# Kernel optimization log

Measured on AMD Instinct MI355X. Metric: run time of the kernel, lower is better.

The kernel has to match this reference:

```python
import jax, jax.numpy as jnp
from jax import lax
import numpy as np

LOG2PI = float(np.log(2.0 * np.pi))
FMIN = float(np.finfo(np.float32).min)


def seq_mask(lengths, maxlen):
    # [B, maxlen] float32
    return (jnp.arange(maxlen)[None] < lengths[:, None]).astype(jnp.float32)


def monotonic_alignment_search(ll, attnmask):
    """Faithful port of GlowTTS.monotonic_alignment_search.
    ll, attnmask: [B, T, S] float32. Returns [B, T, S] float32.
    Note: replicates the source exactly, including stacking backtracked rows
    in descending-j (append) order before masking, as written in the TF code.
    """
    B, T, S = ll.shape
    x_range = jnp.arange(S)[None]  # [1, S]

    def fwd(prob, j_and_ll):
        j, ll_j = j_and_ll  # ll_j: [B, S]
        prev = jnp.pad(prob, ((0, 0), (1, 0)), constant_values=-jnp.inf)[:, :-1]
        max_mask = prob >= prev                       # [B, S] bool
        prob_max = jnp.where(max_mask, prob, prev)
        prob_new = jnp.where(x_range <= j, prob_max + ll_j, FMIN)
        return prob_new, max_mask

    _, direction = lax.scan(fwd, jnp.zeros((B, S), jnp.float32),
                            (jnp.arange(T), jnp.transpose(ll, (1, 0, 2))))
    direction = jnp.transpose(direction, (1, 0, 2)).astype(jnp.int32)  # [B, T, S]
    direction = jnp.where(attnmask.astype(bool), direction, 1)

    index = attnmask[:, 0].sum(axis=-1).astype(jnp.int32) - 1  # [B]
    brange = jnp.arange(B)

    def bwd(index, j):
        attn_j = jax.nn.one_hot(index, S, dtype=jnp.float32)  # drops index<0 like scatter_nd
        d = direction[brange, j, index]                       # [B]
        return index + d - 1, attn_j

    _, attn = lax.scan(bwd, index, jnp.arange(T)[::-1])
    attn = jnp.transpose(attn, (1, 0, 2))  # [B, T, S], rows in append order
    return attn * attnmask


def setup_inputs() -> dict:
    key = jax.random.key(0)
    k1, k2, k3, k4, k5 = jax.random.split(key, 5)
    B, T, S, C = 32, 1200, 384, 160
    latent = jax.random.normal(k1, (B, T, C), dtype=jnp.float32)
    mean = jax.random.normal(k2, (B, S, C), dtype=jnp.float32)
    logdur = jax.random.normal(k3, (B, S), dtype=jnp.float32)
    textlen = jax.random.randint(k4, (B,), S // 2, S + 1).astype(jnp.int32)
    mellen = jax.random.randint(k5, (B,), T // 2, T + 1).astype(jnp.int32)
    return {"latent": latent, "mean": mean, "logdur": logdur,
            "textlen": textlen, "mellen": mellen}


def reference(latent, mean, logdur, textlen, mellen):
    B, T, C = latent.shape
    S = mean.shape[1]
    mask = seq_mask(textlen, S)     # [B, S]
    melmask = seq_mask(mellen, T)   # [B, T]
    attnmask = melmask[..., None] * mask[:, None]  # [B, T, S]

    # pairwise squared distance (cdist via matmul + reduce_sum)
    dist = (jnp.sum(jnp.square(latent), axis=-1, keepdims=True)
            - 2.0 * jnp.einsum('btc,bsc->bts', latent, mean)
            + jnp.sum(jnp.square(mean), axis=-1)[:, None])
    ll = -0.5 * (LOG2PI + dist) * attnmask

    attn = lax.stop_gradient(monotonic_alignment_search(ll, attnmask))
    aligned = jnp.einsum('bts,bsc->btc', attn, mean)  # [B, T, C]

    # negative log-likelihood (dlogdet of the flow omitted: constant here)
    nll = 0.5 * (LOG2PI + jnp.sum(jnp.square(latent - aligned), axis=(1, 2)))
    nll = jnp.mean(nll / (mellen * C).astype(jnp.float32))

    gtdur = jnp.log(jnp.maximum(jnp.sum(attn, axis=1), 1e-05)) * mask
    durloss = jnp.sum(jnp.square(logdur - gtdur), axis=-1) / mellen.astype(jnp.float32)
    durloss = jnp.mean(durloss)

    loss = nll + durloss
    return loss, attn
```

## Files before the change

kernel.cpp:

```cpp
#include <hip/hip_runtime.h>
#include <math.h>

#define LOG2PI 1.8378770664093453f
#define F32MIN (-3.4028234663852886e38f)
#define SMAX 384
#define NW 38

__global__ __launch_bounds__(64) void k_sums(
    const float* __restrict__ latent, const float* __restrict__ mean,
    float* __restrict__ lx2, float* __restrict__ lm2, int BT, int BS, int C) {
  int row = blockIdx.x;
  int lane = threadIdx.x;
  const float* src;
  float* dst;
  if (row < BT) { src = latent + (size_t)row * C; dst = lx2 + row; }
  else          { src = mean + (size_t)(row - BT) * C; dst = lm2 + (row - BT); }
  float s = 0.f;
  for (int c = lane; c < C; c += 64) { float v = src[c]; s += v * v; }
  #pragma unroll
  for (int off = 32; off; off >>= 1) s += __shfl_down(s, off);
  if (lane == 0) *dst = s;
}

__global__ __launch_bounds__(256) void k_scores(
    const float* __restrict__ latent, const float* __restrict__ mean,
    const float* __restrict__ lx2, const float* __restrict__ lm2,
    const int* __restrict__ textlen, const int* __restrict__ mellen,
    float* __restrict__ ll, int T, int S, int C) {
  int b  = blockIdx.z;
  int t0 = blockIdx.x * 64;
  int s0 = blockIdx.y * 64;
  int mel = mellen[b], txt = textlen[b];
  int tid = threadIdx.x;
  int ty = tid >> 4, tx = tid & 15;
  float* out = ll + ((size_t)b * T + t0) * S + s0;

  if (t0 >= mel || s0 >= txt) {
    float4 z = make_float4(0.f, 0.f, 0.f, 0.f);
    #pragma unroll
    for (int i = 0; i < 4; ++i) {
      int tl = ty * 4 + i;
      if (t0 + tl < T) *(float4*)(out + (size_t)tl * S + tx * 4) = z;
    }
    return;
  }

  __shared__ float At[16][64];
  __shared__ float Bt[16][64];
  float acc[4][4] = {};

  const float* Ab = latent + ((size_t)b * T + t0) * C;
  const float* Bb = mean + ((size_t)b * S + s0) * C;

  for (int kk = 0; kk < C; kk += 16) {
    int r  = tid >> 2;
    int cg = tid & 3;
    float4 a = (t0 + r < T) ? *(const float4*)(Ab + (size_t)r * C + kk + cg * 4)
                            : make_float4(0.f, 0.f, 0.f, 0.f);
    float4 bm = *(const float4*)(Bb + (size_t)r * C + kk + cg * 4);
    At[cg * 4 + 0][r] = a.x;  At[cg * 4 + 1][r] = a.y;
    At[cg * 4 + 2][r] = a.z;  At[cg * 4 + 3][r] = a.w;
    Bt[cg * 4 + 0][r] = bm.x; Bt[cg * 4 + 1][r] = bm.y;
    Bt[cg * 4 + 2][r] = bm.z; Bt[cg * 4 + 3][r] = bm.w;
    __syncthreads();
    #pragma unroll
    for (int k = 0; k < 16; ++k) {
      float4 a4 = *(const float4*)&At[k][ty * 4];
      float4 b4 = *(const float4*)&Bt[k][tx * 4];
      float av[4] = {a4.x, a4.y, a4.z, a4.w};
      float bv[4] = {b4.x, b4.y, b4.z, b4.w};
      #pragma unroll
      for (int i = 0; i < 4; ++i)
        #pragma unroll
        for (int j = 0; j < 4; ++j)
          acc[i][j] = fmaf(av[i], bv[j], acc[i][j]);
    }
    __syncthreads();
  }

  #pragma unroll
  for (int i = 0; i < 4; ++i) {
    int t = t0 + ty * 4 + i;
    if (t >= T) continue;
    float lx = lx2[(size_t)b * T + t];
    float4 o;
    float* po = &o.x;
    #pragma unroll
    for (int j = 0; j < 4; ++j) {
      int s = s0 + tx * 4 + j;
      float d = lx - 2.f * acc[i][j] + lm2[(size_t)b * S + s];
      float v = -0.5f * (LOG2PI + d);
      po[j] = (t < mel && s < txt) ? v : 0.f;
    }
    *(float4*)(out + (size_t)(ty * 4 + i) * S + tx * 4) = o;
  }
}

__device__ __forceinline__ float dpp_shr1_neginf(float x) {
  int r = __builtin_amdgcn_update_dpp(
      __float_as_int(-INFINITY), __float_as_int(x),
      0x138 , 0xf, 0xf, false);
  return __int_as_float(r);
}

template <bool MASKED>
__device__ __forceinline__ void mas_step(
    int t, int sbase, int r, const float4 ab, const float2 cc,
    float& p0, float& p1, float& p2, float& p3, float& p4, float& p5,
    unsigned& a0, unsigned& a1, unsigned& a2, unsigned& a3, unsigned& a4,
    unsigned& a5) {
  float l0 = ab.x, l1 = ab.y, l2 = ab.z, l3 = ab.w, l4 = cc.x, l5 = cc.y;
  float pm1 = dpp_shr1_neginf(p5);
  bool c0 = p0 >= pm1, c1 = p1 >= p0, c2 = p2 >= p1;
  bool c3 = p3 >= p2,  c4 = p4 >= p3, c5 = p5 >= p4;
  float m0 = c0 ? p0 : pm1, m1 = c1 ? p1 : p0, m2 = c2 ? p2 : p1;
  float m3 = c3 ? p3 : p2,  m4 = c4 ? p4 : p3, m5 = c5 ? p5 : p4;
  a0 |= (unsigned)c0 << r; a1 |= (unsigned)c1 << r; a2 |= (unsigned)c2 << r;
  a3 |= (unsigned)c3 << r; a4 |= (unsigned)c4 << r; a5 |= (unsigned)c5 << r;
  if (MASKED) {
    p0 = (sbase + 0 <= t) ? m0 + l0 : F32MIN;
    p1 = (sbase + 1 <= t) ? m1 + l1 : F32MIN;
    p2 = (sbase + 2 <= t) ? m2 + l2 : F32MIN;
    p3 = (sbase + 3 <= t) ? m3 + l3 : F32MIN;
    p4 = (sbase + 4 <= t) ? m4 + l4 : F32MIN;
    p5 = (sbase + 5 <= t) ? m5 + l5 : F32MIN;
  } else {
    p0 = m0 + l0; p1 = m1 + l1; p2 = m2 + l2;
    p3 = m3 + l3; p4 = m4 + l4; p5 = m5 + l5;
  }
}

template <int ROWS>
__device__ __forceinline__ void load_chunk_reg(
    float4 (&b4)[32], float2 (&b2)[32],
    const float* __restrict__ llb, int t0, int sbase) {
  #pragma unroll
  for (int r = 0; r < ROWS; ++r) {
    const float* p = llb + (size_t)(t0 + r) * SMAX + sbase;
    b4[r] = *(const float4*)p;
    b2[r] = *(const float2*)(p + 4);
  }
}

template <bool MASKED, int ROWS>
__device__ __forceinline__ void scan_chunk_reg(
    const float4 (&b4)[32], const float2 (&b2)[32], int cw, int sbase,
    float& p0, float& p1, float& p2, float& p3, float& p4, float& p5,
    unsigned* __restrict__ dirT) {
  unsigned a0 = 0, a1 = 0, a2 = 0, a3 = 0, a4 = 0, a5 = 0;
  int t0 = cw * 32;
  #pragma unroll
  for (int r = 0; r < ROWS; ++r) {
    mas_step<MASKED>(t0 + r, sbase, r, b4[r], b2[r],
                     p0, p1, p2, p3, p4, p5, a0, a1, a2, a3, a4, a5);
  }
  unsigned* dcol = dirT + (unsigned)sbase * NW + cw;
  dcol[0] = a0; dcol[NW] = a1; dcol[2 * NW] = a2;
  dcol[3 * NW] = a3; dcol[4 * NW] = a4; dcol[5 * NW] = a5;
}

__global__ __launch_bounds__(64, 1) void k_scan(
    const float* __restrict__ ll, const int* __restrict__ textlen,
    const int* __restrict__ mellen, int* __restrict__ pathidx, int T, int S) {
  int b = blockIdx.x;
  int lane = threadIdx.x;
  __shared__ unsigned dirT[SMAX * NW];

  const float* llb = ll + (size_t)b * T * S;
  int mel = mellen[b], txt = textlen[b];
  int sbase = lane * 6;
  float p0 = 0.f, p1 = 0.f, p2 = 0.f, p3 = 0.f, p4 = 0.f, p5 = 0.f;

  float4 bufA4[32], bufB4[32];
  float2 bufA2[32], bufB2[32];

  load_chunk_reg<32>(bufA4, bufA2, llb, 0, sbase);

  for (int c = 0; c < 12; c += 2) {
    load_chunk_reg<32>(bufB4, bufB2, llb, (c + 1) * 32, sbase);
    scan_chunk_reg<true, 32>(bufA4, bufA2, c, sbase, p0, p1, p2, p3, p4, p5, dirT);
    load_chunk_reg<32>(bufA4, bufA2, llb, (c + 2) * 32, sbase);
    scan_chunk_reg<true, 32>(bufB4, bufB2, c + 1, sbase, p0, p1, p2, p3, p4, p5, dirT);
  }
  for (int c = 12; c < 36; c += 2) {
    load_chunk_reg<32>(bufB4, bufB2, llb, (c + 1) * 32, sbase);
    scan_chunk_reg<false, 32>(bufA4, bufA2, c, sbase, p0, p1, p2, p3, p4, p5, dirT);
    load_chunk_reg<32>(bufA4, bufA2, llb, (c + 2) * 32, sbase);
    scan_chunk_reg<false, 32>(bufB4, bufB2, c + 1, sbase, p0, p1, p2, p3, p4, p5, dirT);
  }
  load_chunk_reg<16>(bufB4, bufB2, llb, 37 * 32, sbase);
  scan_chunk_reg<false, 32>(bufA4, bufA2, 36, sbase, p0, p1, p2, p3, p4, p5, dirT);
  scan_chunk_reg<false, 16>(bufB4, bufB2, 37, sbase, p0, p1, p2, p3, p4, p5, dirT);

  size_t base = (size_t)b * T;
  int k0 = T - mel;
  for (int k = lane; k < k0; k += 64) pathidx[base + k] = txt - 1;

  if (lane == 0) {
    int i = txt - 1;
    int j = mel - 1;
    unsigned w = ~0u;
    bool reload = true;
    for (int k = k0; k < T; ++k) {
      pathidx[base + k] = i;
      if (reload) {
        int ii = (i < 0) ? i + S : i;
        ii = (ii < 0) ? 0 : ii;
        w = (ii < txt) ? dirT[ii * NW + (j >> 5)] : ~0u;
      }
      int d = (int)((w >> (j & 31)) & 1u);
      reload = (d == 0) | ((j & 31) == 0);
      i += d - 1;
      --j;
    }
  }
}

__global__ __launch_bounds__(256) void k_scatter(
    float* __restrict__ attn, const int* __restrict__ pathidx,
    const int* __restrict__ textlen, const int* __restrict__ mellen,
    int B, int T, int S) {
  size_t idx = ((size_t)blockIdx.x * blockDim.x + threadIdx.x) * 4;
  size_t total = (size_t)B * T * S;
  if (idx >= total) return;
  int s = (int)(idx % S);
  size_t row = idx / S;
  int b = (int)(row / T);
  int k = (int)(row % T);
  int pi = pathidx[row];
  int mel = mellen[b], txt = textlen[b];
  float4 o = make_float4(0.f, 0.f, 0.f, 0.f);
  if (k < mel && pi >= 0 && pi < S && pi < txt && pi >= s && pi < s + 4)
    (&o.x)[pi - s] = 1.f;
  *(float4*)(attn + idx) = o;
}

__global__ __launch_bounds__(256) void k_rowloss(
    const float* __restrict__ latent, const float* __restrict__ mean,
    const int* __restrict__ pathidx, const int* __restrict__ textlen,
    const int* __restrict__ mellen, float* __restrict__ rowsum,
    int T, int S, int C) {
  int row = blockIdx.x * 4 + (threadIdx.x >> 6);
  int lane = threadIdx.x & 63;
  int b = row / T, k = row % T;
  int pi = pathidx[row];
  int mel = mellen[b], txt = textlen[b];
  bool on = (k < mel) && (pi >= 0) && (pi < S) && (pi < txt);
  const float* L = latent + (size_t)row * C;
  const float* M = mean + ((size_t)b * S + (on ? pi : 0)) * C;
  float s = 0.f;
  for (int c = lane; c < C; c += 64) {
    float d = L[c] - (on ? M[c] : 0.f);
    s += d * d;
  }
  #pragma unroll
  for (int off = 32; off; off >>= 1) s += __shfl_down(s, off);
  if (lane == 0) rowsum[row] = s;
}

__global__ __launch_bounds__(256) void k_batch(
    const float* __restrict__ rowsum, const int* __restrict__ pathidx,
    const float* __restrict__ logdur, const int* __restrict__ textlen,
    const int* __restrict__ mellen, float* __restrict__ nllc,
    float* __restrict__ durc, int T, int S, int C) {
  int b = blockIdx.x;
  int tid = threadIdx.x;
  __shared__ int hist[512];
  __shared__ float red[256];
  int mel = mellen[b], txt = textlen[b];
  for (int s = tid; s < S; s += 256) hist[s] = 0;
  __syncthreads();
  for (int k = tid; k < T; k += 256) {
    int pi = pathidx[(size_t)b * T + k];
    if (k < mel && pi >= 0 && pi < S && pi < txt) atomicAdd(&hist[pi], 1);
  }
  __syncthreads();
  float part = 0.f;
  for (int s = tid; s < S; s += 256) {
    float cnt = (float)hist[s];
    float gt = logf(fmaxf(cnt, 1e-5f));
    gt = (s < txt) ? gt : 0.f;
    float d = logdur[(size_t)b * S + s] - gt;
    part += d * d;
  }
  red[tid] = part; __syncthreads();
  #pragma unroll
  for (int off = 128; off; off >>= 1) {
    if (tid < off) red[tid] += red[tid + off];
    __syncthreads();
  }
  if (tid == 0) durc[b] = red[0] / (float)mel;
  __syncthreads();
  part = 0.f;
  for (int k = tid; k < T; k += 256) part += rowsum[(size_t)b * T + k];
  red[tid] = part; __syncthreads();
  #pragma unroll
  for (int off = 128; off; off >>= 1) {
    if (tid < off) red[tid] += red[tid + off];
    __syncthreads();
  }
  if (tid == 0) nllc[b] = 0.5f * (LOG2PI + red[0]) / ((float)mel * (float)C);
}

__global__ __launch_bounds__(64) void k_final(
    const float* __restrict__ nllc, const float* __restrict__ durc,
    float* __restrict__ out, int B) {
  int lane = threadIdx.x;
  float v = (lane < B) ? (nllc[lane] + durc[lane]) : 0.f;
  #pragma unroll
  for (int off = 32; off; off >>= 1) v += __shfl_down(v, off);
  if (lane == 0) out[0] = v / (float)B;
}

extern "C" void kernel_launch(void* const* d_in, const int* in_sizes, int n_in,
                              void* d_out, int out_size, void* d_ws, size_t ws_size,
                              hipStream_t stream) {
  (void)n_in; (void)out_size; (void)ws_size;
  const float* latent = (const float*)d_in[0];
  const float* mean   = (const float*)d_in[1];
  const float* logdur = (const float*)d_in[2];
  const int*   textlen = (const int*)d_in[3];
  const int*   mellen  = (const int*)d_in[4];

  int B = in_sizes[3];
  int S = in_sizes[2] / B;
  int C = in_sizes[1] / (B * S);
  int T = in_sizes[0] / (B * C);

  float* out = (float*)d_out;
  float* ll = out + 1;

  char* ws = (char*)d_ws;
  float* lx2    = (float*)ws;
  float* lm2    = lx2 + (size_t)B * T;
  int*   pathidx = (int*)(lm2 + (size_t)B * S);
  float* rowsum  = (float*)(pathidx + (size_t)B * T);
  float* nllc    = rowsum + (size_t)B * T;
  float* durc    = nllc + B;

  k_sums<<<B * T + B * S, 64, 0, stream>>>(latent, mean, lx2, lm2, B * T, B * S, C);

  dim3 g2((T + 63) / 64, (S + 63) / 64, B);
  k_scores<<<g2, 256, 0, stream>>>(latent, mean, lx2, lm2, textlen, mellen, ll, T, S, C);

  k_scan<<<B, 64, 0, stream>>>(ll, textlen, mellen, pathidx, T, S);

  size_t total = (size_t)B * T * S;
  k_scatter<<<(int)((total / 4 + 255) / 256), 256, 0, stream>>>(ll, pathidx, textlen, mellen, B, T, S);

  k_rowloss<<<(B * T) / 4, 256, 0, stream>>>(latent, mean, pathidx, textlen, mellen, rowsum, T, S, C);

  k_batch<<<B, 256, 0, stream>>>(rowsum, pathidx, logdur, textlen, mellen, nllc, durc, T, S, C);

  k_final<<<1, 64, 0, stream>>>(nllc, durc, out, B);
}
```

Measured before the change: 351.4 us.

## Split MAS scan into warp-specialized LDS-staged forward kernel and separate backtrack kernel

The single per-batch scan kernel is replaced by a forward kernel where two producer waves stream ll rows into double-buffered shared memory. One consumer wave interleaves two batches' DP chains to hide latency. Direction bits are computed via sign-bit tricks and fmaxf and written back over the ll buffer in global memory, and a separate backtrack kernel reads them from global. This aims to hide load latency and increase ILP on the serial recurrence, at the cost of half as many blocks, an extra launch, global round-trips for direction bits, and changed tie semantics (p>=prev vs sign of difference, NaN/inf edge cases).

```diff
diff --git a/kernel.cpp b/kernel.cpp
--- a/kernel.cpp
+++ b/kernel.cpp
@@ -4,7 +4,8 @@
 #define LOG2PI 1.8378770664093453f
 #define F32MIN (-3.4028234663852886e38f)
 #define SMAX 384
-#define NW 38
+#define RSTRIDE 392
+#define NCH 75
 
 __global__ __launch_bounds__(64) void k_sums(
     const float* __restrict__ latent, const float* __restrict__ mean,
@@ -103,95 +104,149 @@
   return __int_as_float(r);
 }
 
+struct MasState {
+  float p0, p1, p2, p3, p4, p5;
+  unsigned n0, n1, n2, n3, n4, n5;
+};
+
 template <bool MASKED>
 __device__ __forceinline__ void mas_step(
-    int t, int sbase, int r, const float4 ab, const float2 cc,
-    float& p0, float& p1, float& p2, float& p3, float& p4, float& p5,
-    unsigned& a0, unsigned& a1, unsigned& a2, unsigned& a3, unsigned& a4,
-    unsigned& a5) {
-  float l0 = ab.x, l1 = ab.y, l2 = ab.z, l3 = ab.w, l4 = cc.x, l5 = cc.y;
-  float pm1 = dpp_shr1_neginf(p5);
-  bool c0 = p0 >= pm1, c1 = p1 >= p0, c2 = p2 >= p1;
-  bool c3 = p3 >= p2,  c4 = p4 >= p3, c5 = p5 >= p4;
-  float m0 = c0 ? p0 : pm1, m1 = c1 ? p1 : p0, m2 = c2 ? p2 : p1;
-  float m3 = c3 ? p3 : p2,  m4 = c4 ? p4 : p3, m5 = c5 ? p5 : p4;
-  a0 |= (unsigned)c0 << r; a1 |= (unsigned)c1 << r; a2 |= (unsigned)c2 << r;
-  a3 |= (unsigned)c3 << r; a4 |= (unsigned)c4 << r; a5 |= (unsigned)c5 << r;
+    int t, int sbase, int r, const float2 A0, const float2 A1, const float2 A2,
+    MasState& st) {
+  float l0 = A0.x, l1 = A0.y, l2 = A1.x, l3 = A1.y, l4 = A2.x, l5 = A2.y;
+  float pm1 = dpp_shr1_neginf(st.p5);
+  unsigned s0b = __float_as_uint(st.p0 - pm1)   >> 31;
+  unsigned s1b = __float_as_uint(st.p1 - st.p0) >> 31;
+  unsigned s2b = __float_as_uint(st.p2 - st.p1) >> 31;
+  unsigned s3b = __float_as_uint(st.p3 - st.p2) >> 31;
+  unsigned s4b = __float_as_uint(st.p4 - st.p3) >> 31;
+  unsigned s5b = __float_as_uint(st.p5 - st.p4) >> 31;
+  st.n0 |= s0b << r; st.n1 |= s1b << r; st.n2 |= s2b << r;
+  st.n3 |= s3b << r; st.n4 |= s4b << r; st.n5 |= s5b << r;
+  float v0 = fmaxf(st.p0, pm1) + l0;
+  float v1 = fmaxf(st.p1, st.p0) + l1;
+  float v2 = fmaxf(st.p2, st.p1) + l2;
+  float v3 = fmaxf(st.p3, st.p2) + l3;
+  float v4 = fmaxf(st.p4, st.p3) + l4;
+  float v5 = fmaxf(st.p5, st.p4) + l5;
   if (MASKED) {
-    p0 = (sbase + 0 <= t) ? m0 + l0 : F32MIN;
-    p1 = (sbase + 1 <= t) ? m1 + l1 : F32MIN;
-    p2 = (sbase + 2 <= t) ? m2 + l2 : F32MIN;
-    p3 = (sbase + 3 <= t) ? m3 + l3 : F32MIN;
-    p4 = (sbase + 4 <= t) ? m4 + l4 : F32MIN;
-    p5 = (sbase + 5 <= t) ? m5 + l5 : F32MIN;
+    st.p0 = (sbase + 0 <= t) ? v0 : F32MIN;
+    st.p1 = (sbase + 1 <= t) ? v1 : F32MIN;
+    st.p2 = (sbase + 2 <= t) ? v2 : F32MIN;
+    st.p3 = (sbase + 3 <= t) ? v3 : F32MIN;
+    st.p4 = (sbase + 4 <= t) ? v4 : F32MIN;
+    st.p5 = (sbase + 5 <= t) ? v5 : F32MIN;
   } else {
-    p0 = m0 + l0; p1 = m1 + l1; p2 = m2 + l2;
-    p3 = m3 + l3; p4 = m4 + l4; p5 = m5 + l5;
-  }
-}
-
-template <int ROWS>
-__device__ __forceinline__ void load_chunk_reg(
-    float4 (&b4)[32], float2 (&b2)[32],
-    const float* __restrict__ llb, int t0, int sbase) {
-  #pragma unroll
-  for (int r = 0; r < ROWS; ++r) {
-    const float* p = llb + (size_t)(t0 + r) * SMAX + sbase;
-    b4[r] = *(const float4*)p;
-    b2[r] = *(const float2*)(p + 4);
-  }
-}
-
-template <bool MASKED, int ROWS>
-__device__ __forceinline__ void scan_chunk_reg(
-    const float4 (&b4)[32], const float2 (&b2)[32], int cw, int sbase,
-    float& p0, float& p1, float& p2, float& p3, float& p4, float& p5,
-    unsigned* __restrict__ dirT) {
-  unsigned a0 = 0, a1 = 0, a2 = 0, a3 = 0, a4 = 0, a5 = 0;
-  int t0 = cw * 32;
-  #pragma unroll
-  for (int r = 0; r < ROWS; ++r) {
-    mas_step<MASKED>(t0 + r, sbase, r, b4[r], b2[r],
-                     p0, p1, p2, p3, p4, p5, a0, a1, a2, a3, a4, a5);
-  }
-  unsigned* dcol = dirT + (unsigned)sbase * NW + cw;
-  dcol[0] = a0; dcol[NW] = a1; dcol[2 * NW] = a2;
-  dcol[3 * NW] = a3; dcol[4 * NW] = a4; dcol[5 * NW] = a5;
-}
-
-__global__ __launch_bounds__(64, 1) void k_scan(
-    const float* __restrict__ ll, const int* __restrict__ textlen,
+    st.p0 = v0; st.p1 = v1; st.p2 = v2; st.p3 = v3; st.p4 = v4; st.p5 = v5;
+  }
+}
+
+template <bool MASKED>
+__device__ __forceinline__ void scan_pair16(
+    const float* __restrict__ r0, const float* __restrict__ r1,
+    int t0, int sbase, MasState& s0, MasState& s1) {
+  const float2* qA = (const float2*)(r0 + sbase);
+  const float2* qB = (const float2*)(r1 + sbase);
+  float2 Xa0 = qA[0], Xa1 = qA[1], Xa2 = qA[2];
+  float2 Ya0 = qB[0], Ya1 = qB[1], Ya2 = qB[2];
+  #pragma unroll 1
+  for (int u = 0; u < 16; u += 2) {
+    const float2* pa = qA + (size_t)(u + 1) * (RSTRIDE / 2);
+    float2 Xb0 = pa[0], Xb1 = pa[1], Xb2 = pa[2];
+    const float2* pb = qB + (size_t)(u + 1) * (RSTRIDE / 2);
+    float2 Yb0 = pb[0], Yb1 = pb[1], Yb2 = pb[2];
+    int r = (t0 + u) & 31;
+    mas_step<MASKED>(t0 + u, sbase, r, Xa0, Xa1, Xa2, s0);
+    mas_step<MASKED>(t0 + u, sbase, r, Ya0, Ya1, Ya2, s1);
+    int un = (u + 2 < 16) ? u + 2 : 15;
+    const float2* na = qA + (size_t)un * (RSTRIDE / 2);
+    Xa0 = na[0]; Xa1 = na[1]; Xa2 = na[2];
+    const float2* nb = qB + (size_t)un * (RSTRIDE / 2);
+    Ya0 = nb[0]; Ya1 = nb[1]; Ya2 = nb[2];
+    mas_step<MASKED>(t0 + u + 1, sbase, r + 1, Xb0, Xb1, Xb2, s0);
+    mas_step<MASKED>(t0 + u + 1, sbase, r + 1, Yb0, Yb1, Yb2, s1);
+  }
+}
+
+__device__ __forceinline__ void flush_dir(unsigned* dst, MasState& st) {
+  dst[0] = ~st.n0; dst[1] = ~st.n1; dst[2] = ~st.n2;
+  dst[3] = ~st.n3; dst[4] = ~st.n4; dst[5] = ~st.n5;
+  st.n0 = st.n1 = st.n2 = st.n3 = st.n4 = st.n5 = 0;
+}
+
+__global__ __launch_bounds__(192, 1) void k_fwd(
+    float* llbase, int T, int S) {
+  int pb = blockIdx.x;
+  int tid = threadIdx.x;
+  int lane = tid & 63;
+  int wv = tid >> 6;
+  __shared__ float rows[2][2][17][RSTRIDE];
+
+  if (wv >= 1) {
+    int q = wv - 1;
+    const float* gb = llbase + (size_t)(pb * 2 + q) * T * S;
+    {
+      const float4* g = (const float4*)gb;
+      float4 stg[24];
+      #pragma unroll
+      for (int k = 0; k < 24; ++k) stg[k] = g[k * 64 + lane];
+      #pragma unroll
+      for (int k = 0; k < 24; ++k) {
+        int f = k * 64 + lane;
+        ((float4*)&rows[0][q][f / 96][0])[f % 96] = stg[k];
+      }
+    }
+    __syncthreads();
+    for (int c = 0; c < NCH; ++c) {
+      if (c + 1 < NCH) {
+        const float4* g = (const float4*)(gb + (size_t)(c + 1) * 16 * S);
+        float4 stg[24];
+        #pragma unroll
+        for (int k = 0; k < 24; ++k) stg[k] = g[k * 64 + lane];
+        #pragma unroll
+        for (int k = 0; k < 24; ++k) {
+          int f = k * 64 + lane;
+          ((float4*)&rows[(c + 1) & 1][q][f / 96][0])[f % 96] = stg[k];
+        }
+      }
+      __syncthreads();
+    }
+    return;
+  }
+
+  int sbase = lane * 6;
+  MasState s0 = {0.f,0.f,0.f,0.f,0.f,0.f, 0u,0u,0u,0u,0u,0u};
+  MasState s1 = {0.f,0.f,0.f,0.f,0.f,0.f, 0u,0u,0u,0u,0u,0u};
+  unsigned* dir0 = (unsigned*)(llbase + (size_t)(pb * 2 + 0) * T * S);
+  unsigned* dir1 = (unsigned*)(llbase + (size_t)(pb * 2 + 1) * T * S);
+
+  __syncthreads();
+  for (int c = 0; c < NCH; ++c) {
+    const float* r0 = &rows[c & 1][0][0][0];
+    const float* r1 = &rows[c & 1][1][0][0];
+    int t0 = c * 16;
+    if (c < 24)
+      scan_pair16<true >(r0, r1, t0, sbase, s0, s1);
+    else
+      scan_pair16<false>(r0, r1, t0, sbase, s0, s1);
+    if (c & 1) {
+      int w = c >> 1;
+      flush_dir(dir0 + (size_t)w * S + sbase, s0);
+      flush_dir(dir1 + (size_t)w * S + sbase, s1);
+    }
+    __syncthreads();
+  }
+  flush_dir(dir0 + (size_t)37 * S + sbase, s0);
+  flush_dir(dir1 + (size_t)37 * S + sbase, s1);
+}
+
+__global__ __launch_bounds__(64) void k_bwd(
+    const float* llbase, const int* __restrict__ textlen,
     const int* __restrict__ mellen, int* __restrict__ pathidx, int T, int S) {
   int b = blockIdx.x;
   int lane = threadIdx.x;
-  __shared__ unsigned dirT[SMAX * NW];
-
-  const float* llb = ll + (size_t)b * T * S;
   int mel = mellen[b], txt = textlen[b];
-  int sbase = lane * 6;
-  float p0 = 0.f, p1 = 0.f, p2 = 0.f, p3 = 0.f, p4 = 0.f, p5 = 0.f;
-
-  float4 bufA4[32], bufB4[32];
-  float2 bufA2[32], bufB2[32];
-
-  load_chunk_reg<32>(bufA4, bufA2, llb, 0, sbase);
-
-  for (int c = 0; c < 12; c += 2) {
-    load_chunk_reg<32>(bufB4, bufB2, llb, (c + 1) * 32, sbase);
-    scan_chunk_reg<true, 32>(bufA4, bufA2, c, sbase, p0, p1, p2, p3, p4, p5, dirT);
-    load_chunk_reg<32>(bufA4, bufA2, llb, (c + 2) * 32, sbase);
-    scan_chunk_reg<true, 32>(bufB4, bufB2, c + 1, sbase, p0, p1, p2, p3, p4, p5, dirT);
-  }
-  for (int c = 12; c < 36; c += 2) {
-    load_chunk_reg<32>(bufB4, bufB2, llb, (c + 1) * 32, sbase);
-    scan_chunk_reg<false, 32>(bufA4, bufA2, c, sbase, p0, p1, p2, p3, p4, p5, dirT);
-    load_chunk_reg<32>(bufA4, bufA2, llb, (c + 2) * 32, sbase);
-    scan_chunk_reg<false, 32>(bufB4, bufB2, c + 1, sbase, p0, p1, p2, p3, p4, p5, dirT);
-  }
-  load_chunk_reg<16>(bufB4, bufB2, llb, 37 * 32, sbase);
-  scan_chunk_reg<false, 32>(bufA4, bufA2, 36, sbase, p0, p1, p2, p3, p4, p5, dirT);
-  scan_chunk_reg<false, 16>(bufB4, bufB2, 37, sbase, p0, p1, p2, p3, p4, p5, dirT);
-
+  const unsigned* dirg = (const unsigned*)(llbase + (size_t)b * T * S);
   size_t base = (size_t)b * T;
   int k0 = T - mel;
   for (int k = lane; k < k0; k += 64) pathidx[base + k] = txt - 1;
@@ -206,7 +261,7 @@
       if (reload) {
         int ii = (i < 0) ? i + S : i;
         ii = (ii < 0) ? 0 : ii;
-        w = (ii < txt) ? dirT[ii * NW + (j >> 5)] : ~0u;
+        w = (ii < txt) ? dirg[(size_t)(j >> 5) * S + ii] : ~0u;
       }
       int d = (int)((w >> (j & 31)) & 1u);
       reload = (d == 0) | ((j & 31) == 0);
@@ -343,7 +398,9 @@
   dim3 g2((T + 63) / 64, (S + 63) / 64, B);
   k_scores<<<g2, 256, 0, stream>>>(latent, mean, lx2, lm2, textlen, mellen, ll, T, S, C);
 
-  k_scan<<<B, 64, 0, stream>>>(ll, textlen, mellen, pathidx, T, S);
+  k_fwd<<<B / 2, 192, 0, stream>>>(ll, T, S);
+
+  k_bwd<<<B, 64, 0, stream>>>(ll, textlen, mellen, pathidx, T, S);
 
   size_t total = (size_t)B * T * S;
   k_scatter<<<(int)((total / 4 + 255) / 256), 256, 0, stream>>>(ll, pathidx, textlen, mellen, B, T, S);
```

Measured after the change: 440.1 us. 25.2% more time.
